# Kernel tuning notes

Measured on AMD Instinct MI355X. Metric: run time of the kernel, lower is better.

The kernel has to match this reference:

```python
import jax, jax.numpy as jnp
import numpy as np

B, C, H, W = 2, 2048, 64, 64
C4, C16 = C // 4, C // 16  # 512, 128


def conv1x1(x, w, b):
    # x: [B,Cin,H,W], w: [Cout,Cin]
    return jnp.einsum('bchw,oc->bohw', x, w) + b[None, :, None, None]


def conv3x3(x, w, b):
    # w: [Cout,Cin,3,3]
    y = jax.lax.conv_general_dilated(
        x, w, window_strides=(1, 1), padding='SAME',
        dimension_numbers=('NCHW', 'OIHW', 'NCHW'))
    return y + b[None, :, None, None]


def bn_relu(x, s, t):
    # inference BatchNorm folded to per-channel affine, then ReLU
    return jax.nn.relu(x * s[None, :, None, None] + t[None, :, None, None])


def setup_inputs() -> dict:
    key = jax.random.key(0)
    ks = jax.random.split(key, 32)
    n = lambda k, shp, s=0.02: (jax.random.normal(k, shp, jnp.float32) * s)
    inp = {
        'x': jax.random.normal(ks[0], (B, C, H, W), jnp.float32),
        # position branch
        'wq_p': n(ks[1], (C16, C)), 'bq_p': n(ks[2], (C16,)),
        'wpc': n(ks[3], (C4, C)), 'bpc': n(ks[4], (C4,)),
        'spc': 1.0 + n(ks[5], (C4,)), 'tpc': n(ks[6], (C4,)),
        'wk': n(ks[7], (C16, C4)), 'bk': n(ks[8], (C16,)),
        'wv': n(ks[9], (C4, C)), 'bv': n(ks[10], (C4,)),
        'wrp': n(ks[11], (C4, C)), 'brp': n(ks[12], (C4,)),
        'srp': 1.0 + n(ks[13], (C4,)), 'trp': n(ks[14], (C4,)),
        'wpf': n(ks[15], (C4, C4, 3, 3)), 'bpf': n(ks[16], (C4,)),
        'spf': 1.0 + n(ks[17], (C4,)), 'tpf': n(ks[18], (C4,)),
        'gamma_p': jax.random.normal(ks[19], (1,), jnp.float32) * 0.1,
        # channel branch
        'wq_c': n(ks[20], (C4, C)), 'bq_c': n(ks[21], (C4,)),
        'wrc': n(ks[22], (C4, C)), 'brc': n(ks[23], (C4,)),
        'src': 1.0 + n(ks[24], (C4,)), 'trc': n(ks[25], (C4,)),
        'wcf': n(ks[26], (C4, C4, 3, 3)), 'bcf': n(ks[27], (C4,)),
        'scf': 1.0 + n(ks[28], (C4,)), 'tcf': n(ks[29], (C4,)),
        'gamma_c': jax.random.normal(ks[30], (1,), jnp.float32) * 0.1,
    }
    return inp


def reference(x, wq_p, bq_p, wpc, bpc, spc, tpc, wk, bk, wv, bv,
              wrp, brp, srp, trp, wpf, bpf, spf, tpf, gamma_p,
              wq_c, bq_c, wrc, brc, src, trc, wcf, bcf, scf, tcf, gamma_c):
    Bn, Cc, Hh, Ww = x.shape
    N = Hh * Ww
    # ---- position attention ----
    q_p = conv1x1(x, wq_p, bq_p).reshape(Bn, -1, N)           # [B,C/16,N]
    pc_feat = bn_relu(conv1x1(x, wpc, bpc), spc, tpc)          # [B,C/4,H,W]
    k_p = conv1x1(pc_feat, wk, bk).reshape(Bn, -1, N)          # [B,C/16,N]
    attn_p = jax.nn.softmax(jnp.einsum('bcn,bcm->bnm', q_p, k_p), axis=-1)  # [B,N,N]
    v_p = conv1x1(x, wv, bv).reshape(Bn, -1, N)                # [B,C/4,N]
    out_p = jnp.einsum('bcm,bnm->bcn', v_p, attn_p).reshape(Bn, -1, Hh, Ww)
    out_p = gamma_p * out_p + bn_relu(conv1x1(x, wrp, brp), srp, trp)
    out_p = bn_relu(conv3x3(out_p, wpf, bpf), spf, tpf)        # [B,C/4,H,W]
    # ---- channel attention ----
    q_c = conv1x1(x, wq_c, bq_c).reshape(Bn, -1, N)            # [B,C/4,N]
    k_c = pc_feat.reshape(Bn, -1, N)                           # [B,C/4,N]
    energy = jnp.einsum('bcn,bdn->bcd', q_c, k_c)              # [B,C/4,C/4]
    energy_new = jnp.max(energy, axis=-1, keepdims=True) - energy
    attn_c = jax.nn.softmax(energy_new, axis=-1)
    v_c = out_p.reshape(Bn, -1, N)
    out_c = jnp.einsum('bcd,bdn->bcn', attn_c, v_c).reshape(Bn, -1, Hh, Ww)
    out_c = gamma_c * out_c + bn_relu(conv1x1(x, wrc, brc), src, trc)
    out_c = bn_relu(conv3x3(out_c, wcf, bcf), scf, tcf)
    return (out_c, out_p)
```

## Files before the change

### kernel.cpp

```cpp
#include <hip/hip_runtime.h>
#include <hip/hip_bf16.h>
#include <stdint.h>

typedef unsigned short u16;
typedef short bf16x8 __attribute__((ext_vector_type(8)));
typedef float f32x4 __attribute__((ext_vector_type(4)));

#define DEV static __device__ __forceinline__

DEV float b2f(u16 u) { return __uint_as_float(((unsigned)u) << 16); }
DEV u16 f2bu(float x) {
  union { __hip_bfloat16 h; u16 u; } c;
  c.h = __float2bfloat16(x);
  return c.u;
}

DEV void gload16(const void* g, void* l) {
  __builtin_amdgcn_global_load_lds(
      (const __attribute__((address_space(1))) void*)(uintptr_t)g,
      (__attribute__((address_space(3))) void*)(uintptr_t)l, 16, 0, 0);
}

struct Epi {
  const float* bias;
  const float* alpha_ptr;
  const u16* add;
  long ld_add, add_bs;
  int relu;
  u16* outb; long ldo;  long outb_bs;
  int padrow;
  u16* outt; long ldot; long outt_bs;
  int padmap;
  float* outf; long ldof; long outf_bs;
  float* outu;
  int mode;
  u16 *f_qT, *f_pc, *f_pcT, *f_vp, *f_rpT, *f_qc, *f_rc;
};

template <int BN>
__global__ __launch_bounds__(256) void gemm_bt(
    const u16* __restrict__ A, long lda, long a_bs,
    const u16* __restrict__ Bt, long ldb, long b_bs,
    int K, int conv9, int zdiv, Epi e)
{
  constexpr int FN = BN / 32;
  constexpr int SLOT = 4096 + BN * 32;
  __shared__ u16 SMEM[3 * SLOT];

  const int bz = blockIdx.z;
  int batch = bz, ksteps = K >> 5, ksbase = 0;
  if (zdiv > 1) {
    batch = bz / zdiv;
    int sl = bz - batch * zdiv;
    ksteps = (K / zdiv) >> 5;
    ksbase = sl * ksteps;
  }
  const int gx = gridDim.x, gy = gridDim.y;
  const int nwg = gx * gy;
  const int orig = blockIdx.y * gx + blockIdx.x;
  const int q8 = nwg >> 3, r8 = nwg & 7;
  const int xcd = orig & 7, lid = orig >> 3;
  const int wgid = (xcd < r8 ? xcd * (q8 + 1) : r8 * (q8 + 1) + (xcd - r8) * q8) + lid;
  const int GROUP = 8;
  const int span = GROUP * gy;
  const int group_id = wgid / span;
  const int first_m = group_id * GROUP;
  const int gsz = (GROUP < gx - first_m) ? GROUP : (gx - first_m);
  const int rem = wgid - group_id * span;
  const int bm = first_m + rem % gsz;
  const int bn = rem / gsz;

  const u16* Ab = A + (long)batch * a_bs;
  const u16* Bb = Bt + (long)batch * b_bs;
  const int m0 = bm * 128;
  const int n0 = bn * BN;
  const int t = threadIdx.x;
  const int w = t >> 6, l = t & 63;
  const int wr = w >> 1, wc = w & 1;
  const int lr = l & 15, lg = l >> 4;

  f32x4 acc[4][FN];
#pragma unroll
  for (int i = 0; i < 4; ++i)
#pragma unroll
    for (int j = 0; j < FN; ++j) acc[i][j] = (f32x4){0.f, 0.f, 0.f, 0.f};

  auto stage = [&](int ks, int slot) {
    u16* As = SMEM + slot * SLOT;
    u16* Bs = As + 4096;
    const int k0 = ks << 5;
    long brow = 0;
    int bk0 = k0;
    if (conv9) {
      int s = k0 >> 9;
      int kh = s / 3, kw = s - kh * 3;
      brow = (long)((kh - 1) * 66 + (kw - 1));
      bk0 = k0 & 511;
    }
#pragma unroll
    for (int r = 0; r < 2; ++r) {
      int idx = (r << 8) + t;
      int row = idx >> 2;
      int ko = (((idx & 3) ^ ((row >> 1) & 3)) << 3);
      gload16(Ab + (long)(m0 + row) * lda + (k0 + ko),
              (char*)As + (((r << 8) + (t & 192)) << 4));
    }
#pragma unroll
    for (int r = 0; r < BN / 64; ++r) {
      int idx = (r << 8) + t;
      int row = idx >> 2;
      int ko = (((idx & 3) ^ ((row >> 1) & 3)) << 3);
      gload16(Bb + ((long)(n0 + row) + brow) * ldb + (bk0 + ko),
              (char*)Bs + (((r << 8) + (t & 192)) << 4));
    }
  };

  auto compute = [&](int slot) {
    const u16* As = SMEM + slot * SLOT;
    const u16* Bs = As + 4096;
    __builtin_amdgcn_s_setprio(1);
    bf16x8 af[4], bfr[FN];
#pragma unroll
    for (int i = 0; i < 4; ++i) {
      int row = wr * 64 + i * 16 + lr;
      int cg = lg ^ ((row >> 1) & 3);
      af[i] = *(const bf16x8*)(As + row * 32 + cg * 8);
    }
#pragma unroll
    for (int j = 0; j < FN; ++j) {
      int row = wc * (BN / 2) + j * 16 + lr;
      int cg = lg ^ ((row >> 1) & 3);
      bfr[j] = *(const bf16x8*)(Bs + row * 32 + cg * 8);
    }
#pragma unroll
    for (int i = 0; i < 4; ++i)
#pragma unroll
      for (int j = 0; j < FN; ++j)
        acc[i][j] = __builtin_amdgcn_mfma_f32_16x16x32_bf16(af[i], bfr[j], acc[i][j], 0, 0, 0);
    __builtin_amdgcn_s_setprio(0);
  };

  const int nk = ksteps;
  stage(ksbase, 0);
  if (nk > 1) stage(ksbase + 1, 1);
  for (int tt = 0; tt < nk; ++tt) {
    if (tt < nk - 1) {
      if constexpr (BN == 128) asm volatile("s_waitcnt vmcnt(4)" ::: "memory");
      else                     asm volatile("s_waitcnt vmcnt(3)" ::: "memory");
    } else {
      asm volatile("s_waitcnt vmcnt(0)" ::: "memory");
    }
    __builtin_amdgcn_s_barrier();
    if (tt + 2 < nk) stage(ksbase + tt + 2, (tt + 2) % 3);
    compute(tt % 3);
    asm volatile("s_waitcnt lgkmcnt(0)" ::: "memory");
  }

  const float alpha = e.alpha_ptr ? e.alpha_ptr[0] : 1.0f;

  if (e.mode == 1) {
    const int seg = (m0 < 128) ? 0 : (m0 < 640) ? 1 : (m0 < 1152) ? 2 :
                    (m0 < 1664) ? 3 : (m0 < 2176) ? 4 : 5;
    const bool doT = (seg == 0 || seg == 1 || seg == 3);
    if (doT) __syncthreads();
#pragma unroll
    for (int i = 0; i < 4; ++i) {
#pragma unroll
      for (int j = 0; j < FN; ++j) {
        const int gn = n0 + wc * (BN / 2) + j * 16 + lr;
#pragma unroll
        for (int q = 0; q < 4; ++q) {
          const int gm = m0 + wr * 64 + i * 16 + lg * 4 + q;
          float v = acc[i][j][q] + e.bias[gm];
          const int gnl = gn - n0, gml = gm - m0;
          if (seg == 0) {
            SMEM[gnl * 128 + (((gml >> 3) ^ (gnl & 7)) << 3) + (gml & 7)] = f2bu(v);
          } else if (seg == 1) {
            v = fmaxf(v, 0.f);
            u16 bb = f2bu(v);
            e.f_pc[((long)batch * 512 + (gm - 128)) * 4096 + gn] = bb;
            SMEM[gnl * 128 + (((gml >> 3) ^ (gnl & 7)) << 3) + (gml & 7)] = bb;
          } else if (seg == 2) {
            e.f_vp[((long)batch * 512 + (gm - 640)) * 4096 + gn] = f2bu(v);
          } else if (seg == 3) {
            v = fmaxf(v, 0.f);
            SMEM[gnl * 128 + (((gml >> 3) ^ (gnl & 7)) << 3) + (gml & 7)] = f2bu(v);
          } else if (seg == 4) {
            e.f_qc[((long)batch * 512 + (gm - 1664)) * 4096 + gn] = f2bu(v);
          } else {
            v = fmaxf(v, 0.f);
            e.f_rc[((long)batch * 512 + (gm - 2176)) * 4096 + gn] = f2bu(v);
          }
        }
      }
    }
    if (doT) {
      __syncthreads();
      u16* dst; long ld;
      if (seg == 0)      { dst = e.f_qT  + ((long)batch * 4096 + n0) * 128;                ld = 128; }
      else if (seg == 1) { dst = e.f_pcT + ((long)batch * 4096 + n0) * 512 + (m0 - 128);   ld = 512; }
      else               { dst = e.f_rpT + ((long)batch * 4096 + n0) * 512 + (m0 - 1152);  ld = 512; }
#pragma unroll
      for (int k = 0; k < 8; ++k) {
        int chunk = (k << 8) + t;
        int row = chunk >> 4, c16 = chunk & 15;
        bf16x8 vv = *(const bf16x8*)(SMEM + row * 128 + ((c16 ^ (row & 7)) << 3));
        *(bf16x8*)(dst + (long)row * ld + c16 * 8) = vv;
      }
    }
    return;
  }

  if (e.mode == 2) {
    __syncthreads();
#pragma unroll
    for (int i = 0; i < 4; ++i) {
#pragma unroll
      for (int j = 0; j < FN; ++j) {
        const int gn = n0 + wc * (BN / 2) + j * 16 + lr;
#pragma unroll
        for (int q = 0; q < 4; ++q) {
          const int gm = m0 + wr * 64 + i * 16 + lg * 4 + q;
          float v = acc[i][j][q] * alpha +
                    b2f(e.add[(long)batch * e.add_bs + (long)gm * e.ld_add + gn]);
          const int gnl = gn - n0, gml = gm - m0;
          SMEM[gnl * 128 + (((gml >> 3) ^ (gnl & 7)) << 3) + (gml & 7)] = f2bu(v);
        }
      }
    }
    __syncthreads();
#pragma unroll
    for (int k = 0; k < BN / 16; ++k) {
      int chunk = (k << 8) + t;
      int row = chunk >> 4, c16 = chunk & 15;
      int gnr = n0 + row;
      long rowo = (long)((gnr >> 6) + 1) * 66 + (gnr & 63) + 1;
      bf16x8 vv = *(const bf16x8*)(SMEM + row * 128 + ((c16 ^ (row & 7)) << 3));
      *(bf16x8*)(e.outt + (long)batch * e.outt_bs + rowo * e.ldot + m0 + c16 * 8) = vv;
    }
    return;
  }

  if (e.mode == 3) {
    __syncthreads();
#pragma unroll
    for (int i = 0; i < 4; ++i) {
#pragma unroll
      for (int j = 0; j < FN; ++j) {
        const int gn = n0 + wc * (BN / 2) + j * 16 + lr;
#pragma unroll
        for (int q = 0; q < 4; ++q) {
          const int gm = m0 + wr * 64 + i * 16 + lg * 4 + q;
          float v = fmaxf(acc[i][j][q] + e.bias[gm], 0.f);
          int ph = gn / 66, pw = gn - ph * 66;
          if (ph >= 1 && ph <= 64 && pw >= 1 && pw <= 64)
            e.outu[(long)batch * 2097152 + (long)gm * 4096 + (ph - 1) * 64 + (pw - 1)] = v;
          const int gnl = gn - n0, gml = gm - m0;
          SMEM[gnl * 128 + (((gml >> 3) ^ (gnl & 7)) << 3) + (gml & 7)] = f2bu(v);
        }
      }
    }
    __syncthreads();
#pragma unroll
    for (int k = 0; k < BN / 16; ++k) {
      int chunk = (k << 8) + t;
      int row = chunk >> 4, c16 = chunk & 15;
      int gnr = n0 + row;
      int ph = gnr / 66, pw = gnr - ph * 66;
      if (ph >= 1 && ph <= 64 && pw >= 1 && pw <= 64) {
        long nn = (long)(ph - 1) * 64 + (pw - 1);
        bf16x8 vv = *(const bf16x8*)(SMEM + row * 128 + ((c16 ^ (row & 7)) << 3));
        *(bf16x8*)(e.outt + ((long)batch * 4096 + nn) * 512 + m0 + c16 * 8) = vv;
      }
    }
    return;
  }

#pragma unroll
  for (int i = 0; i < 4; ++i) {
#pragma unroll
    for (int j = 0; j < FN; ++j) {
      const int gn = n0 + wc * (BN / 2) + j * 16 + lr;
#pragma unroll
      for (int q = 0; q < 4; ++q) {
        const int gm = m0 + wr * 64 + i * 16 + lg * 4 + q;
        float v = acc[i][j][q] * alpha;
        if (e.bias) v += e.bias[gm];
        if (e.add) v += b2f(e.add[(long)batch * e.add_bs + (long)gm * e.ld_add + gn]);
        if (e.relu) v = fmaxf(v, 0.f);
        if (e.outb) {
          long rowo = gm;
          if (e.padrow) rowo = (long)((gm >> 6) + 1) * 66 + (gm & 63) + 1;
          e.outb[(long)batch * e.outb_bs + rowo * e.ldo + gn] = f2bu(v);
        }
        if (e.outf)
          e.outf[(long)bz * e.outf_bs + (long)gm * e.ldof + gn] = v;
        if (e.outu) {
          int ph = gn / 66, pw = gn - ph * 66;
          if (ph >= 1 && ph <= 64 && pw >= 1 && pw <= 64)
            e.outu[(long)batch * 2097152 + (long)gm * 4096 + (ph - 1) * 64 + (pw - 1)] = v;
        }
        if (e.outt) {
          long rt = gn;
          if (e.padmap) rt = (long)((gn >> 6) + 1) * 66 + (gn & 63) + 1;
          e.outt[(long)batch * e.outt_bs + rt * e.ldot + gm] = f2bu(v);
        }
      }
    }
  }
}

__global__ __launch_bounds__(512, 2) void k_flash(
    const u16* __restrict__ qT, const u16* __restrict__ kT,
    const u16* __restrict__ vp,
    u16* __restrict__ opart,
    float* __restrict__ lpart)
{
  __shared__ u16 kt_lds[2][64 * 128];
  __shared__ u16 p_lds[128 * 64];

  const int orig = blockIdx.x;
  const int xcd = orig & 7;
  const int qtile = orig >> 3;
  const int split = xcd & 3;
  const int b = xcd >> 2;

  const int t = threadIdx.x;
  const int w = t >> 6;
  const int l = t & 63;
  const int lr = l & 15, lg = l >> 4;
  const int n0 = qtile * 128;
  const int m_base = split * 1024;

  const u16* qb = qT + ((long)b * 4096 + n0 + w * 16) * 128;
  const u16* kb = kT + ((long)b * 4096 + m_base) * 128;

  bf16x8 qf[4];
#pragma unroll
  for (int ks = 0; ks < 4; ++ks)
    qf[ks] = *(const bf16x8*)(qb + (long)lr * 128 + ks * 32 + lg * 8);

  f32x4 acc[8][4];
#pragma unroll
  for (int i = 0; i < 8; ++i)
#pragma unroll
    for (int j = 0; j < 4; ++j) acc[i][j] = (f32x4){0.f, 0.f, 0.f, 0.f};
  float lrun[4] = {0.f, 0.f, 0.f, 0.f};

  auto stage = [&](int mt, int buf) {
#pragma unroll
    for (int r = 0; r < 2; ++r) {
      int idx = (r << 9) + t;
      int row = idx >> 4;
      int g = idx & 15;
      int gs = g ^ (row & 7);
      gload16(kb + ((long)(mt * 64 + row)) * 128 + gs * 8,
              (char*)(&kt_lds[buf][0]) + (((r << 9) + (t & 448)) << 4));
    }
  };

  stage(0, 0);
  __syncthreads();

  const int nt = 16;
  for (int mt = 0; mt < nt; ++mt) {
    const int cur = mt & 1;
    if (mt + 1 < nt) stage(mt + 1, cur ^ 1);

    bf16x8 vv[4][2];
#pragma unroll
    for (int cs = 0; cs < 4; ++cs) {
#pragma unroll
      for (int k2 = 0; k2 < 2; ++k2) {
        const u16* va = vp + ((long)b * 512 + w * 64 + cs * 16 + lr) * 4096 +
                        m_base + mt * 64 + k2 * 32 + lg * 8;
        vv[cs][k2] = *(const bf16x8*)va;
      }
    }

    f32x4 sacc[4];
#pragma unroll
    for (int ms = 0; ms < 4; ++ms) sacc[ms] = (f32x4){0.f, 0.f, 0.f, 0.f};
#pragma unroll
    for (int ms = 0; ms < 4; ++ms) {
#pragma unroll
      for (int ks = 0; ks < 4; ++ks) {
        int row = ms * 16 + lr;
        int gs = (ks * 4 + lg) ^ (row & 7);
        bf16x8 kf = *(const bf16x8*)(&kt_lds[cur][0] + row * 128 + gs * 8);
        sacc[ms] = __builtin_amdgcn_mfma_f32_16x16x32_bf16(qf[ks], kf, sacc[ms], 0, 0, 0);
      }
    }

    float rs[4] = {0.f, 0.f, 0.f, 0.f};
#pragma unroll
    for (int ms = 0; ms < 4; ++ms) {
#pragma unroll
      for (int q = 0; q < 4; ++q) {
        float p = __expf(sacc[ms][q]);
        rs[q] += p;
        int prow = w * 16 + 4 * lg + q;
        int m = ms * 16 + lr;
        int gm = m >> 3, offm = m & 7;
        int gsm = gm ^ (prow & 7);
        p_lds[prow * 64 + gsm * 8 + offm] = f2bu(p);
      }
    }
#pragma unroll
    for (int q = 0; q < 4; ++q) {
      rs[q] += __shfl_xor(rs[q], 1);
      rs[q] += __shfl_xor(rs[q], 2);
      rs[q] += __shfl_xor(rs[q], 4);
      rs[q] += __shfl_xor(rs[q], 8);
      lrun[q] += rs[q];
    }

    __syncthreads();

    __builtin_amdgcn_s_setprio(1);
#pragma unroll
    for (int ntl = 0; ntl < 8; ++ntl) {
      int row = ntl * 16 + lr;
      int gs0 = (0 * 4 + lg) ^ (row & 7);
      int gs1 = (1 * 4 + lg) ^ (row & 7);
      bf16x8 pf0 = *(const bf16x8*)(&p_lds[0] + row * 64 + gs0 * 8);
      bf16x8 pf1 = *(const bf16x8*)(&p_lds[0] + row * 64 + gs1 * 8);
#pragma unroll
      for (int cs = 0; cs < 4; ++cs) {
        acc[ntl][cs] = __builtin_amdgcn_mfma_f32_16x16x32_bf16(pf0, vv[cs][0], acc[ntl][cs], 0, 0, 0);
        acc[ntl][cs] = __builtin_amdgcn_mfma_f32_16x16x32_bf16(pf1, vv[cs][1], acc[ntl][cs], 0, 0, 0);
      }
    }
    __builtin_amdgcn_s_setprio(0);
    __syncthreads();
  }

  const long pbase = ((long)split * 2 + b) * 4096;
  if (lr == 0) {
#pragma unroll
    for (int q = 0; q < 4; ++q)
      lpart[pbase + n0 + w * 16 + 4 * lg + q] = lrun[q];
  }
#pragma unroll
  for (int ntl = 0; ntl < 8; ++ntl) {
#pragma unroll
    for (int cs = 0; cs < 4; ++cs) {
#pragma unroll
      for (int q = 0; q < 4; ++q) {
        long row = n0 + ntl * 16 + 4 * lg + q;
        int col = w * 64 + cs * 16 + lr;
        opart[(pbase + row) * 512 + col] = f2bu(acc[ntl][cs][q]);
      }
    }
  }
}

__global__ __launch_bounds__(256) void k_combine_p(
    const u16* __restrict__ opart, const float* __restrict__ lpart,
    const u16* __restrict__ rpT, const float* __restrict__ gamma_p,
    u16* __restrict__ padi)
{
  const int t = threadIdx.x;
  const long rg = (long)blockIdx.x * 4 + (t >> 6);
  const int b = (int)(rg >> 12), n = (int)(rg & 4095);
  const int l = t & 63;
  const int c0 = l * 8;
  float lsum = 0.f;
#pragma unroll
  for (int s = 0; s < 4; ++s) lsum += lpart[((long)s * 2 + b) * 4096 + n];
  float o[8];
#pragma unroll
  for (int i = 0; i < 8; ++i) o[i] = 0.f;
#pragma unroll
  for (int s = 0; s < 4; ++s) {
    const u16* op = opart + ((((long)s * 2 + b) * 4096 + n) * 512) + c0;
    bf16x8 a = *(const bf16x8*)op;
#pragma unroll
    for (int i = 0; i < 8; ++i) o[i] += b2f((u16)a[i]);
  }
  const float g = gamma_p[0];
  const float inv = 1.0f / lsum;
  bf16x8 rv = *(const bf16x8*)(rpT + ((long)b * 4096 + n) * 512 + c0);
  bf16x8 outv;
#pragma unroll
  for (int i = 0; i < 8; ++i)
    outv[i] = (short)f2bu(g * o[i] * inv + b2f((u16)rv[i]));
  const int h = n >> 6, ww = n & 63;
  *(bf16x8*)(padi + ((long)b * 4736 + (long)(h + 1) * 66 + ww + 1) * 512 + c0) = outv;
}

__global__ __launch_bounds__(256) void k_transpose_x(const float* __restrict__ x,
                                                     u16* __restrict__ xt) {
  __shared__ float tile[64][65];
  const int b = blockIdx.z;
  const int c0 = blockIdx.x * 64;
  const int n0 = blockIdx.y * 64;
  const int t = threadIdx.x;
  const int tn = t & 63, tc = t >> 6;
  const float* xp = x + ((long)b * 2048 + c0) * 4096 + n0;
#pragma unroll
  for (int i = 0; i < 16; ++i)
    tile[tc + i * 4][tn] = xp[(long)(tc + i * 4) * 4096 + tn];
  __syncthreads();
  u16* xo = xt + ((long)b * 4096 + n0) * 2048 + c0;
  const int oc = t & 63, on = t >> 6;
#pragma unroll
  for (int i = 0; i < 16; ++i)
    xo[(long)(on + i * 4) * 2048 + oc] = f2bu(tile[oc][on + i * 4]);
}

__global__ void k_prep(const float* wq_p, const float* wpc, const float* spc,
                       const float* wv, const float* wrp, const float* srp,
                       const float* wq_c, const float* wrc, const float* src_,
                       const float* wk, const float* wpf, const float* spf,
                       const float* wcf, const float* scf,
                       const float* bq_p, const float* bpc, const float* tpc,
                       const float* bv, const float* brp, const float* trp,
                       const float* bq_c, const float* brc, const float* trc,
                       const float* bpf, const float* tpf,
                       const float* bcf, const float* tcf,
                       u16* wall, u16* wpfb, u16* wcfb, u16* wkb,
                       float* biasAll, float* biasPF, float* biasCF) {
  const long W = 2688L * 2048;
  const long W3 = 512L * 512 * 9;
  const long TOT = W + 2 * W3 + 65536 + 3712;
  for (long i = (long)blockIdx.x * 256 + threadIdx.x; i < TOT; i += (long)gridDim.x * 256) {
    if (i < W) {
      int r = (int)(i >> 11), c = (int)(i & 2047);
      float v;
      if (r < 128) v = wq_p[(long)r * 2048 + c];
      else if (r < 640)  { int rr = r - 128;  v = spc[rr] * wpc[(long)rr * 2048 + c]; }
      else if (r < 1152) { int rr = r - 640;  v = wv[(long)rr * 2048 + c]; }
      else if (r < 1664) { int rr = r - 1152; v = srp[rr] * wrp[(long)rr * 2048 + c]; }
      else if (r < 2176) { int rr = r - 1664; v = wq_c[(long)rr * 2048 + c]; }
      else               { int rr = r - 2176; v = src_[rr] * wrc[(long)rr * 2048 + c]; }
      wall[i] = f2bu(v);
    } else if (i < W + 2 * W3) {
      int which = (i < W + W3) ? 0 : 1;
      long j = i - W - (long)which * W3;
      int o = (int)(j / (512 * 9));
      long rem = j - (long)o * (512 * 9);
      int khw = (int)(rem >> 9);
      int c = (int)(rem & 511);
      int kh = khw / 3, kw = khw - kh * 3;
      const float* wsrc = which ? wcf : wpf;
      const float* ssrc = which ? scf : spf;
      u16* dst = which ? wcfb : wpfb;
      dst[j] = f2bu(ssrc[o] * wsrc[(((long)o * 512 + c) * 3 + kh) * 3 + kw]);
    } else if (i < W + 2 * W3 + 65536) {
      long j = i - W - 2 * W3;
      wkb[j] = f2bu(wk[j]);
    } else {
      long j = i - W - 2 * W3 - 65536;
      if (j < 2688) {
        int r = (int)j;
        float v;
        if (r < 128) v = bq_p[r];
        else if (r < 640)  { int k = r - 128;  v = spc[k] * bpc[k] + tpc[k]; }
        else if (r < 1152) { int k = r - 640;  v = bv[k]; }
        else if (r < 1664) { int k = r - 1152; v = srp[k] * brp[k] + trp[k]; }
        else if (r < 2176) { int k = r - 1664; v = bq_c[k]; }
        else               { int k = r - 2176; v = src_[k] * brc[k] + trc[k]; }
        biasAll[r] = v;
      } else if (j < 3200) {
        int k = (int)(j - 2688);
        biasPF[k] = spf[k] * bpf[k] + tpf[k];
      } else {
        int k = (int)(j - 3200);
        biasCF[k] = scf[k] * bcf[k] + tcf[k];
      }
    }
  }
}

__global__ void k_softmax_chan(const float* __restrict__ EP, u16* __restrict__ A) {
  const long row = blockIdx.x;
  const int batch = (int)(row >> 9), r = (int)(row & 511);
  const int l = threadIdx.x;
  float v[8];
#pragma unroll
  for (int i = 0; i < 8; ++i) v[i] = 0.f;
  for (int s = 0; s < 4; ++s) {
    const float* e = EP + (((long)batch * 4 + s) * 512 + r) * 512 + l * 8;
#pragma unroll
    for (int i = 0; i < 8; ++i) v[i] += e[i];
  }
  float mn = 1e30f;
#pragma unroll
  for (int i = 0; i < 8; ++i) mn = fminf(mn, v[i]);
  for (int o = 32; o > 0; o >>= 1) mn = fminf(mn, __shfl_xor(mn, o));
  float s = 0.f;
#pragma unroll
  for (int i = 0; i < 8; ++i) { v[i] = __expf(mn - v[i]); s += v[i]; }
  for (int o = 32; o > 0; o >>= 1) s += __shfl_xor(s, o);
  const float inv = 1.0f / s;
  u16* out = A + row * 512;
#pragma unroll
  for (int i = 0; i < 8; ++i) out[l * 8 + i] = f2bu(v[i] * inv);
}

extern "C" void kernel_launch(void* const* d_in, const int* in_sizes, int n_in,
                              void* d_out, int out_size, void* d_ws, size_t ws_size,
                              hipStream_t stream) {
  (void)in_sizes; (void)n_in; (void)out_size;
  const float* x     = (const float*)d_in[0];
  const float* wq_p  = (const float*)d_in[1];
  const float* bq_p  = (const float*)d_in[2];
  const float* wpc   = (const float*)d_in[3];
  const float* bpc   = (const float*)d_in[4];
  const float* spc   = (const float*)d_in[5];
  const float* tpc   = (const float*)d_in[6];
  const float* wk    = (const float*)d_in[7];
  const float* wv    = (const float*)d_in[9];
  const float* bv    = (const float*)d_in[10];
  const float* wrp   = (const float*)d_in[11];
  const float* brp   = (const float*)d_in[12];
  const float* srp   = (const float*)d_in[13];
  const float* trp   = (const float*)d_in[14];
  const float* wpf   = (const float*)d_in[15];
  const float* bpf   = (const float*)d_in[16];
  const float* spf   = (const float*)d_in[17];
  const float* tpf   = (const float*)d_in[18];
  const float* gamma_p = (const float*)d_in[19];
  const float* wq_c  = (const float*)d_in[20];
  const float* bq_c  = (const float*)d_in[21];
  const float* wrc   = (const float*)d_in[22];
  const float* brc   = (const float*)d_in[23];
  const float* src_  = (const float*)d_in[24];
  const float* trc   = (const float*)d_in[25];
  const float* wcf   = (const float*)d_in[26];
  const float* bcf   = (const float*)d_in[27];
  const float* scf   = (const float*)d_in[28];
  const float* tcf   = (const float*)d_in[29];
  const float* gamma_c = (const float*)d_in[30];

  float* outc = (float*)d_out;
  float* outp = outc + 4194304;

  if (ws_size < 151000000ULL) return;

  char* ws = (char*)d_ws;
  size_t off = 0;
  auto alloc = [&](size_t sz) { void* p = ws + off; off += (sz + 255) & ~(size_t)255; return p; };

  char* region0 = (char*)alloc(67108864);
  u16* xbT     = (u16*)region0;
  u16* Wall    = (u16*)(region0 + 33554432);
  u16* wkb     = (u16*)(region0 + 44564480);
  u16* opart   = (u16*)region0;
  u16* wpfb  = (u16*)alloc(4718592);
  u16* wcfb  = (u16*)alloc(4718592);
  float* biasAll = (float*)alloc(2688 * 4);
  float* biasPF  = (float*)alloc(2048);
  float* biasCF  = (float*)alloc(2048);
  u16* qT   = (u16*)alloc(2097152);
  u16* pc   = (u16*)alloc(8388608);
  u16* pcT  = (u16*)alloc(8388608);
  u16* vp   = (u16*)alloc(8388608);
  u16* rpT  = (u16*)alloc(8388608);
  u16* qc   = (u16*)alloc(8388608);
  u16* rc   = (u16*)alloc(8388608);
  u16* kT   = (u16*)alloc(2097152);
  u16* pad  = (u16*)alloc((size_t)2 * 4736 * 512 * 2);
  u16* vcT  = (u16*)alloc(8388608);
  u16* attnc = (u16*)alloc(1048576);
  float* lpart = (float*)alloc(131072);
  float* epart = (float*)pcT;

  const dim3 blk(256);

  hipMemsetAsync(pad, 0, (size_t)2 * 4736 * 512 * 2, stream);
  k_transpose_x<<<dim3(32, 64, 2), blk, 0, stream>>>(x, xbT);
  k_prep<<<dim3(2048), blk, 0, stream>>>(wq_p, wpc, spc, wv, wrp, srp, wq_c, wrc, src_,
                                         wk, wpf, spf, wcf, scf,
                                         bq_p, bpc, tpc, bv, brp, trp, bq_c, brc, trc,
                                         bpf, tpf, bcf, tcf,
                                         Wall, wpfb, wcfb, wkb, biasAll, biasPF, biasCF);

  {
    Epi e{}; e.bias = biasAll; e.mode = 1;
    e.f_qT = qT; e.f_pc = pc; e.f_pcT = pcT; e.f_vp = vp; e.f_rpT = rpT; e.f_qc = qc; e.f_rc = rc;
    gemm_bt<128><<<dim3(21, 32, 2), blk, 0, stream>>>(Wall, 2048, 0, xbT, 2048, 4096L * 2048,
                                                      2048, 0, 1, e);
  }

  {
    Epi e{}; e.outb = kT; e.ldo = 128; e.outb_bs = 4096L * 128;
    gemm_bt<64><<<dim3(32, 2, 2), blk, 0, stream>>>(pcT, 512, 4096L * 512, wkb, 512, 0,
                                                    512, 0, 1, e);
  }

  k_flash<<<dim3(256), dim3(512), 0, stream>>>(qT, kT, vp, opart, lpart);
  k_combine_p<<<dim3(2048), blk, 0, stream>>>(opart, lpart, rpT, gamma_p, pad + 128 * 512);

  {
    Epi e{}; e.bias = biasPF; e.mode = 3; e.outu = outp; e.outt = vcT;
    gemm_bt<128><<<dim3(4, 35, 2), blk, 0, stream>>>(wpfb, 4608, 0, pad + 128 * 512, 512,
                                                     4736L * 512, 4608, 1, 1, e);
  }

  {
    Epi e{}; e.outf = epart; e.ldof = 512; e.outf_bs = 512L * 512;
    gemm_bt<64><<<dim3(4, 8, 8), blk, 0, stream>>>(qc, 4096, 512L * 4096, pc, 4096, 512L * 4096,
                                                   4096, 0, 4, e);
  }
  k_softmax_chan<<<dim3(1024), dim3(64), 0, stream>>>(epart, attnc);

  {
    Epi e{}; e.alpha_ptr = gamma_c; e.mode = 2;
    e.add = rc; e.ld_add = 4096; e.add_bs = 512L * 4096;
    e.outt = pad + 128 * 512; e.ldot = 512; e.outt_bs = 4736L * 512;
    gemm_bt<128><<<dim3(4, 32, 2), blk, 0, stream>>>(attnc, 512, 512L * 512, vcT, 512, 4096L * 512,
                                                     512, 0, 1, e);
  }

  {
    Epi e{}; e.bias = biasCF; e.relu = 1; e.outu = outc;
    gemm_bt<128><<<dim3(4, 35, 2), blk, 0, stream>>>(wcfb, 4608, 0, pad + 128 * 512, 512,
                                                     4736L * 512, 4608, 1, 1, e);
  }
}
```

Baseline: 486.2 us.

## Split-K the two 3x3 conv GEMMs and reduce partials in separate combine kernels

```diff
diff --git a/kernel.cpp b/kernel.cpp
--- a/kernel.cpp
+++ b/kernel.cpp
@@ -32,7 +32,6 @@
   u16* outt; long ldot; long outt_bs;
   int padmap;
   float* outf; long ldof; long outf_bs;
-  float* outu;
   int mode;
   u16 *f_qT, *f_pc, *f_pcT, *f_vp, *f_rpT, *f_qc, *f_rc;
 };
@@ -241,41 +240,6 @@
     return;
   }
 
-  if (e.mode == 3) {
-    __syncthreads();
-#pragma unroll
-    for (int i = 0; i < 4; ++i) {
-#pragma unroll
-      for (int j = 0; j < FN; ++j) {
-        const int gn = n0 + wc * (BN / 2) + j * 16 + lr;
-#pragma unroll
-        for (int q = 0; q < 4; ++q) {
-          const int gm = m0 + wr * 64 + i * 16 + lg * 4 + q;
-          float v = fmaxf(acc[i][j][q] + e.bias[gm], 0.f);
-          int ph = gn / 66, pw = gn - ph * 66;
-          if (ph >= 1 && ph <= 64 && pw >= 1 && pw <= 64)
-            e.outu[(long)batch * 2097152 + (long)gm * 4096 + (ph - 1) * 64 + (pw - 1)] = v;
-          const int gnl = gn - n0, gml = gm - m0;
-          SMEM[gnl * 128 + (((gml >> 3) ^ (gnl & 7)) << 3) + (gml & 7)] = f2bu(v);
-        }
-      }
-    }
-    __syncthreads();
-#pragma unroll
-    for (int k = 0; k < BN / 16; ++k) {
-      int chunk = (k << 8) + t;
-      int row = chunk >> 4, c16 = chunk & 15;
-      int gnr = n0 + row;
-      int ph = gnr / 66, pw = gnr - ph * 66;
-      if (ph >= 1 && ph <= 64 && pw >= 1 && pw <= 64) {
-        long nn = (long)(ph - 1) * 64 + (pw - 1);
-        bf16x8 vv = *(const bf16x8*)(SMEM + row * 128 + ((c16 ^ (row & 7)) << 3));
-        *(bf16x8*)(e.outt + ((long)batch * 4096 + nn) * 512 + m0 + c16 * 8) = vv;
-      }
-    }
-    return;
-  }
-
 #pragma unroll
   for (int i = 0; i < 4; ++i) {
 #pragma unroll
@@ -295,11 +259,6 @@
         }
         if (e.outf)
           e.outf[(long)bz * e.outf_bs + (long)gm * e.ldof + gn] = v;
-        if (e.outu) {
-          int ph = gn / 66, pw = gn - ph * 66;
-          if (ph >= 1 && ph <= 64 && pw >= 1 && pw <= 64)
-            e.outu[(long)batch * 2097152 + (long)gm * 4096 + (ph - 1) * 64 + (pw - 1)] = v;
-        }
         if (e.outt) {
           long rt = gn;
           if (e.padmap) rt = (long)((gn >> 6) + 1) * 66 + (gn & 63) + 1;
@@ -487,6 +446,53 @@
     outv[i] = (short)f2bu(g * o[i] * inv + b2f((u16)rv[i]));
   const int h = n >> 6, ww = n & 63;
   *(bf16x8*)(padi + ((long)b * 4736 + (long)(h + 1) * 66 + ww + 1) * 512 + c0) = outv;
+}
+
+__global__ __launch_bounds__(256) void k_combine_c1(
+    const float* __restrict__ part,
+    const float* __restrict__ biasPF,
+    float* __restrict__ outp, u16* __restrict__ vct)
+{
+  __shared__ short tile[64][65];
+  const int b = blockIdx.z;
+  const int n0 = blockIdx.x * 64;
+  const int c0 = blockIdx.y * 64;
+  const int t = threadIdx.x;
+  const int tn = t & 63, tc4 = t >> 6;
+  const int h = n0 >> 6;
+  const long npbase = (long)(h + 1) * 66 + 1;
+  const float* p0 = part + ((long)(b * 2 + 0) * 512) * 4480;
+  const float* p1 = part + ((long)(b * 2 + 1) * 512) * 4480;
+#pragma unroll
+  for (int i = 0; i < 16; ++i) {
+    int c = c0 + tc4 + i * 4;
+    long idx = (long)c * 4480 + npbase + tn;
+    float v = fmaxf(p0[idx] + p1[idx] + biasPF[c], 0.f);
+    outp[((long)b * 512 + c) * 4096 + n0 + tn] = v;
+    tile[tc4 + i * 4][tn] = (short)f2bu(v);
+  }
+  __syncthreads();
+  const int cc = t & 63, nn4 = t >> 6;
+#pragma unroll
+  for (int i = 0; i < 16; ++i) {
+    int n = n0 + nn4 + i * 4;
+    vct[((long)b * 4096 + n) * 512 + c0 + cc] = (u16)tile[cc][nn4 + i * 4];
+  }
+}
+
+__global__ void k_combine_c2(const float* __restrict__ part,
+                             const float* __restrict__ biasCF,
+                             float* __restrict__ outc) {
+  long i = (long)blockIdx.x * 256 + threadIdx.x;
+  if (i >= 4194304L) return;
+  int n = (int)(i & 4095);
+  long bc = i >> 12;
+  int b = (int)(bc >> 9), c = (int)(bc & 511);
+  int h = n >> 6, w_ = n & 63;
+  long pos = (long)(h + 1) * 66 + w_ + 1;
+  long i0 = ((long)(b * 2 + 0) * 512 + c) * 4480 + pos;
+  long i1 = ((long)(b * 2 + 1) * 512 + c) * 4480 + pos;
+  outc[i] = fmaxf(part[i0] + part[i1] + biasCF[c], 0.f);
 }
 
 __global__ __launch_bounds__(256) void k_transpose_x(const float* __restrict__ x,
@@ -648,6 +654,7 @@
   u16* Wall    = (u16*)(region0 + 33554432);
   u16* wkb     = (u16*)(region0 + 44564480);
   u16* opart   = (u16*)region0;
+  float* cpart = (float*)region0;
   u16* wpfb  = (u16*)alloc(4718592);
   u16* wcfb  = (u16*)alloc(4718592);
   float* biasAll = (float*)alloc(2688 * 4);
@@ -694,10 +701,11 @@
   k_combine_p<<<dim3(2048), blk, 0, stream>>>(opart, lpart, rpT, gamma_p, pad + 128 * 512);
 
   {
-    Epi e{}; e.bias = biasPF; e.mode = 3; e.outu = outp; e.outt = vcT;
-    gemm_bt<128><<<dim3(4, 35, 2), blk, 0, stream>>>(wpfb, 4608, 0, pad + 128 * 512, 512,
-                                                     4736L * 512, 4608, 1, 1, e);
-  }
+    Epi e{}; e.outf = cpart; e.ldof = 4480; e.outf_bs = 512L * 4480;
+    gemm_bt<128><<<dim3(4, 35, 4), blk, 0, stream>>>(wpfb, 4608, 0, pad + 128 * 512, 512,
+                                                     4736L * 512, 4608, 1, 2, e);
+  }
+  k_combine_c1<<<dim3(64, 8, 2), blk, 0, stream>>>(cpart, biasPF, outp, vcT);
 
   {
     Epi e{}; e.outf = epart; e.ldof = 512; e.outf_bs = 512L * 512;
@@ -715,8 +723,9 @@
   }
 
   {
-    Epi e{}; e.bias = biasCF; e.relu = 1; e.outu = outc;
-    gemm_bt<128><<<dim3(4, 35, 2), blk, 0, stream>>>(wcfb, 4608, 0, pad + 128 * 512, 512,
-                                                     4736L * 512, 4608, 1, 1, e);
-  }
-}
+    Epi e{}; e.outf = cpart; e.ldof = 4480; e.outf_bs = 512L * 4480;
+    gemm_bt<128><<<dim3(4, 35, 4), blk, 0, stream>>>(wcfb, 4608, 0, pad + 128 * 512, 512,
+                                                     4736L * 512, 4608, 1, 2, e);
+  }
+  k_combine_c2<<<dim3(16384), blk, 0, stream>>>(cpart, biasCF, outc);
+}
```

Result: slower. 510.3 us (+5.0%).
